# Kernel tuning notes

Hardware: AMD Instinct MI355X
Metric: run time of the kernel (lower is better)

The kernel has to match this reference:

```python
import jax, jax.numpy as jnp
import numpy as np

EPS = 1e-6  # torch F.pairwise_distance eps: dist = ||a - b + eps||_2


def pairwise_distance(feature):
    # Faithful to torch.nn.functional.pairwise_distance(a, b, p=2, eps=1e-6):
    # d_ij = sqrt( sum_k (a_k - b_k + eps)^2 )
    #      = sqrt( ||a||^2 + ||b||^2 - 2 a.b + 2*eps*(sum(a)-sum(b)) + d*eps^2 )
    d = feature.shape[1]
    sq = jnp.sum(feature * feature, axis=1)          # [N]
    s = jnp.sum(feature, axis=1)                     # [N]
    gram = feature @ feature.T                       # [N, N] GEMM
    d2 = (sq[:, None] + sq[None, :] - 2.0 * gram
          + 2.0 * EPS * (s[:, None] - s[None, :]) + d * EPS * EPS)
    return jnp.sqrt(jnp.maximum(d2, 0.0))


def setup_inputs() -> dict:
    key = jax.random.key(0)
    k1, k2 = jax.random.split(key)
    N, D, K = 8192, 512, 64
    feature = jax.random.normal(k1, (N, D), dtype=jnp.float32)
    centroid_ids = jax.random.randint(k2, (K,), 0, N, dtype=jnp.int64 if jax.config.jax_enable_x64 else jnp.int32)
    return {"feature": feature, "centroid_ids": centroid_ids}


def reference(feature, centroid_ids):
    N = feature.shape[0]
    K = centroid_ids.shape[0]
    pd = pairwise_distance(feature)                   # [N, N]
    # gather distances to centroids: torch.gather(pd, 1, centroid_ids.repeat(N,1))
    dc = pd[:, centroid_ids]                          # [N, K]
    # compute_facility_energy: -sum_i min_k d(i, centroid_k)
    facility_energy = -jnp.sum(jnp.min(dc, axis=1))
    # get_cluster_assignment
    predictions = jnp.argmin(dc, axis=1).astype(jnp.float32)   # [N]
    mask = jnp.zeros((N,), jnp.float32).at[centroid_ids].set(1.0)
    constraint_vect = jnp.zeros((N,), jnp.float32).at[centroid_ids].set(
        jnp.arange(K, dtype=jnp.float32))
    y_fixed = (1.0 - mask) * predictions + constraint_vect
    return facility_energy, y_fixed
```

## Files before the change

kernel.cpp:

```cpp
#include <hip/hip_runtime.h>

typedef unsigned long long u64;

#define NPTS 8192
#define DIM  512
#define NK   64
#define BM   128
#define KP   8
#define KD   64
#define NT   (NPTS/BM)
#define ALP  132
#define BLP  68

#define WS_DOT  0
#define WS_STAT (KP * NK * NPTS)

__global__ __launch_bounds__(256) void gemm_kernel(
    const float* __restrict__ f, const int* __restrict__ cid,
    float* __restrict__ ws, float* __restrict__ out)
{
    __shared__ float Al[KD * ALP];
    __shared__ float Bl[KD * BLP];

    const int t     = threadIdx.x;
    const int tile  = blockIdx.x & (NT - 1);
    const int kp    = blockIdx.x >> 6;
    const int kbase = kp * KD;
    if (blockIdx.x == 0 && t == 0) out[0] = 0.f;

    {
        const int srow = t >> 1, half = t & 1;
        const float* fr = f + (size_t)(tile * BM + srow) * DIM + kbase + half * 32;
        float s = 0.f, q = 0.f;
        #pragma unroll
        for (int j = 0; j < 8; ++j) {
            float4 v = *(const float4*)(fr + 4 * j);
            s += (v.x + v.y) + (v.z + v.w);
            q = fmaf(v.x, v.x, q); q = fmaf(v.y, v.y, q);
            q = fmaf(v.z, v.z, q); q = fmaf(v.w, v.w, q);
            const int k0 = half * 32 + 4 * j;
            Al[(k0+0) * ALP + srow] = v.x;
            Al[(k0+1) * ALP + srow] = v.y;
            Al[(k0+2) * ALP + srow] = v.z;
            Al[(k0+3) * ALP + srow] = v.w;
        }
        s += __shfl_xor(s, 1);
        q += __shfl_xor(q, 1);
        if (half == 0)
            ((float2*)(ws + WS_STAT))[(size_t)kp * NPTS + tile * BM + srow] =
                make_float2(s, q);
    }
    {
        const int col = t & 63, qg = t >> 6;
        const float* gb = f + (size_t)cid[col] * DIM + kbase + qg * 16;
        #pragma unroll
        for (int j = 0; j < 4; ++j) {
            float4 v = *(const float4*)(gb + 4 * j);
            const int k0 = qg * 16 + 4 * j;
            Bl[(k0+0) * BLP + col] = v.x;
            Bl[(k0+1) * BLP + col] = v.y;
            Bl[(k0+2) * BLP + col] = v.z;
            Bl[(k0+3) * BLP + col] = v.w;
        }
    }
    __syncthreads();

    const int rg = t & 15;
    const int cg = t >> 4;
    float acc[8][4];
    #pragma unroll
    for (int i = 0; i < 8; ++i)
        #pragma unroll
        for (int c = 0; c < 4; ++c) acc[i][c] = 0.f;

    #pragma unroll 8
    for (int k = 0; k < KD; ++k) {
        const float4 a0 = *(const float4*)&Al[k * ALP + 4 * rg];
        const float4 a1 = *(const float4*)&Al[k * ALP + 64 + 4 * rg];
        const float4 b0 = *(const float4*)&Bl[k * BLP + 4 * cg];
        const float av[8] = {a0.x, a0.y, a0.z, a0.w, a1.x, a1.y, a1.z, a1.w};
        #pragma unroll
        for (int i = 0; i < 8; ++i) {
            acc[i][0] = fmaf(av[i], b0.x, acc[i][0]);
            acc[i][1] = fmaf(av[i], b0.y, acc[i][1]);
            acc[i][2] = fmaf(av[i], b0.z, acc[i][2]);
            acc[i][3] = fmaf(av[i], b0.w, acc[i][3]);
        }
    }

    const int pbase = tile * BM + 4 * rg;
    #pragma unroll
    for (int c = 0; c < 4; ++c) {
        float* d0 = ws + WS_DOT + (size_t)(kp * NK + 4 * cg + c) * NPTS + pbase;
        *(float4*)(d0)      = make_float4(acc[0][c], acc[1][c], acc[2][c], acc[3][c]);
        *(float4*)(d0 + 64) = make_float4(acc[4][c], acc[5][c], acc[6][c], acc[7][c]);
    }
}

__global__ __launch_bounds__(512) void epi_kernel(
    const float* __restrict__ ws, const int* __restrict__ cid,
    float* __restrict__ out)
{
    __shared__ u64   keys[4][BM];
    __shared__ float cqL[NK], csL[NK];
    __shared__ int   cidL[NK];
    __shared__ float ener[2];

    const int t    = threadIdx.x;
    const int p    = t & 127;
    const int j    = t >> 7;
    const int tile = blockIdx.x;
    const int gi   = tile * BM + p;
    const float2* st = (const float2*)(ws + WS_STAT);

    if (t < NK) {
        const int cr = cid[t];
        float s = 0.f, q = 0.f;
        #pragma unroll
        for (int kp = 0; kp < KP; ++kp) {
            float2 v = st[(size_t)kp * NPTS + cr]; s += v.x; q += v.y;
        }
        cqL[t] = q; csL[t] = s; cidL[t] = cr;
    }
    float s = 0.f, q = 0.f;
    #pragma unroll
    for (int kp = 0; kp < KP; ++kp) {
        float2 v = st[(size_t)kp * NPTS + gi]; s += v.x; q += v.y;
    }
    __syncthreads();

    u64 key = ~0ull;
    #pragma unroll 4
    for (int c = 0; c < 16; ++c) {
        const int col = j * 16 + c;
        float dot = 0.f;
        #pragma unroll
        for (int kp = 0; kp < KP; ++kp)
            dot += ws[WS_DOT + (size_t)(kp * NK + col) * NPTS + gi];
        float d2 = q + cqL[col] - 2.f * dot + 2.0e-6f * (s - csL[col])
                 + 5.12e-10f;
        float dist = sqrtf(fmaxf(d2, 0.f));
        u64 kk = (((u64)__float_as_uint(dist)) << 6) | (unsigned)col;
        key = (kk < key) ? kk : key;
    }
    keys[j][p] = key;
    __syncthreads();

    if (t < BM) {
        u64 kmin = keys[0][t];
        #pragma unroll
        for (int g = 1; g < 4; ++g) {
            u64 o = keys[g][t];
            kmin = (o < kmin) ? o : kmin;
        }
        const int gp = tile * BM + t;
        float y = (float)(unsigned)(kmin & 63ull);
        for (int k = 0; k < NK; ++k)
            if (cidL[k] == gp) y = (float)k;
        out[1 + gp] = y;
        float e = __uint_as_float((unsigned)(kmin >> 6));
        #pragma unroll
        for (int off = 32; off; off >>= 1) e += __shfl_xor(e, off);
        if ((t & 63) == 0) ener[t >> 6] = e;
    }
    __syncthreads();
    if (t == 0) atomicAdd(out, -(ener[0] + ener[1]));
}

extern "C" void kernel_launch(void* const* d_in, const int* in_sizes, int n_in,
                              void* d_out, int out_size, void* d_ws, size_t ws_size,
                              hipStream_t stream) {
    const float* f   = (const float*)d_in[0];
    const int*   cid = (const int*)d_in[1];
    float*       out = (float*)d_out;
    float*       ws  = (float*)d_ws;

    gemm_kernel<<<NT * KP, 256, 0, stream>>>(f, cid, ws, out);
    epi_kernel<<<NT, 512, 0, stream>>>(ws, cid, out);
}
```

Measured before the change: 26.50 us.

## Use 8x8 register tiles with split-K across thread halves and LDS reduction

Each thread now computes an 8x8 output tile over half of the K chunk instead of a 4x8 tile over the full chunk. The two thread halves combine their partial sums through shared memory before one half writes results. The goal is more FMAs per LDS load (higher arithmetic intensity). The cost is more accumulator registers, an extra barrier, a 64-value LDS round trip, and half the threads idle during the final write.

```diff
diff --git a/kernel.cpp b/kernel.cpp
--- a/kernel.cpp
+++ b/kernel.cpp
@@ -11,6 +11,7 @@
 #define NT   (NPTS/BM)
 #define ALP  132
 #define BLP  68
+#define CMP  132
 
 #define WS_DOT  0
 #define WS_STAT (KP * NK * NPTS)
@@ -65,35 +66,53 @@
     }
     __syncthreads();
 
-    const int rg = t & 15;
-    const int cg = t >> 4;
-    float acc[8][4];
+    const int u    = t & 127;
+    const int kh   = t >> 7;
+    const int rowg = u >> 3;
+    const int colg = u & 7;
+    float acc[8][8];
     #pragma unroll
     for (int i = 0; i < 8; ++i)
         #pragma unroll
-        for (int c = 0; c < 4; ++c) acc[i][c] = 0.f;
+        for (int c = 0; c < 8; ++c) acc[i][c] = 0.f;
 
     #pragma unroll 8
-    for (int k = 0; k < KD; ++k) {
-        const float4 a0 = *(const float4*)&Al[k * ALP + 4 * rg];
-        const float4 a1 = *(const float4*)&Al[k * ALP + 64 + 4 * rg];
-        const float4 b0 = *(const float4*)&Bl[k * BLP + 4 * cg];
+    for (int kk = 0; kk < 32; ++kk) {
+        const int k = kh * 32 + kk;
+        const float4 a0 = *(const float4*)&Al[k * ALP + 8 * rowg];
+        const float4 a1 = *(const float4*)&Al[k * ALP + 8 * rowg + 4];
+        const float4 b0 = *(const float4*)&Bl[k * BLP + 8 * colg];
+        const float4 b1 = *(const float4*)&Bl[k * BLP + 8 * colg + 4];
         const float av[8] = {a0.x, a0.y, a0.z, a0.w, a1.x, a1.y, a1.z, a1.w};
+        const float bv[8] = {b0.x, b0.y, b0.z, b0.w, b1.x, b1.y, b1.z, b1.w};
         #pragma unroll
-        for (int i = 0; i < 8; ++i) {
-            acc[i][0] = fmaf(av[i], b0.x, acc[i][0]);
-            acc[i][1] = fmaf(av[i], b0.y, acc[i][1]);
-            acc[i][2] = fmaf(av[i], b0.z, acc[i][2]);
-            acc[i][3] = fmaf(av[i], b0.w, acc[i][3]);
+        for (int i = 0; i < 8; ++i)
+            #pragma unroll
+            for (int c = 0; c < 8; ++c)
+                acc[i][c] = fmaf(av[i], bv[c], acc[i][c]);
+    }
+    __syncthreads();
+
+    float* Comb = Al;
+    if (kh == 1) {
+        #pragma unroll
+        for (int v = 0; v < 64; ++v)
+            Comb[v * CMP + u] = acc[v >> 3][v & 7];
+    }
+    __syncthreads();
+    if (kh == 0) {
+        #pragma unroll
+        for (int v = 0; v < 64; ++v)
+            acc[v >> 3][v & 7] += Comb[v * CMP + u];
+
+        const int pbase = tile * BM + 8 * rowg;
+        #pragma unroll
+        for (int c = 0; c < 8; ++c) {
+            float* d0 = ws + WS_DOT
+                      + (size_t)(kp * NK + 8 * colg + c) * NPTS + pbase;
+            *(float4*)(d0)     = make_float4(acc[0][c], acc[1][c], acc[2][c], acc[3][c]);
+            *(float4*)(d0 + 4) = make_float4(acc[4][c], acc[5][c], acc[6][c], acc[7][c]);
         }
-    }
-
-    const int pbase = tile * BM + 4 * rg;
-    #pragma unroll
-    for (int c = 0; c < 4; ++c) {
-        float* d0 = ws + WS_DOT + (size_t)(kp * NK + 4 * cg + c) * NPTS + pbase;
-        *(float4*)(d0)      = make_float4(acc[0][c], acc[1][c], acc[2][c], acc[3][c]);
-        *(float4*)(d0 + 64) = make_float4(acc[4][c], acc[5][c], acc[6][c], acc[7][c]);
     }
 }
 
```

Measured after the change: 27.82 us. 5.0% more time.
